# Optimization experiments

Hardware: AMD Instinct MI355X
Metric: run time of the kernel (lower is better)

Reference implementation:

```python
import jax, jax.numpy as jnp
import numpy as np

N = 50000      # num nodes
E = 800000     # num edges (avg degree 16)
IN = 128       # raw node feature dim
H = 64         # h_dim
L = 2          # num_conv
K = 5          # negative_rate
EPS = 1e-3     # keras BatchNormalization default epsilon


def setup_inputs() -> dict:
    key = jax.random.key(0)
    ks = jax.random.split(key, 12)
    node_feat = jax.random.normal(ks[0], (N, IN), dtype=jnp.float32)
    emb_w = jax.random.normal(ks[1], (IN, H), dtype=jnp.float32) * 0.05
    emb_b = jnp.zeros((H,), dtype=jnp.float32)
    conv_w = jax.random.normal(ks[2], (L, 2 * H, H), dtype=jnp.float32) * 0.05
    conv_b = jnp.zeros((L, H), dtype=jnp.float32)
    bn_gamma = 1.0 + 0.1 * jax.random.normal(ks[3], (L, H), dtype=jnp.float32)
    bn_beta = 0.1 * jax.random.normal(ks[4], (L, H), dtype=jnp.float32)
    bn_mean = 0.1 * jax.random.normal(ks[5], (L, H), dtype=jnp.float32)
    bn_var = jax.random.uniform(ks[6], (L, H), dtype=jnp.float32, minval=0.5, maxval=1.5)
    w_relation = jax.random.normal(ks[7], (1, H), dtype=jnp.float32) * 0.05
    src = jax.random.randint(ks[8], (E,), 0, N, dtype=jnp.int32)
    dst = jax.random.randint(ks[9], (E,), 0, N, dtype=jnp.int32)
    neg_dst = jax.random.randint(ks[10], (E * K,), 0, N, dtype=jnp.int32)
    return dict(node_feat=node_feat, emb_w=emb_w, emb_b=emb_b, conv_w=conv_w,
                conv_b=conv_b, bn_gamma=bn_gamma, bn_beta=bn_beta,
                bn_mean=bn_mean, bn_var=bn_var, w_relation=w_relation,
                src=src, dst=dst, neg_dst=neg_dst)


def reference(node_feat, emb_w, emb_b, conv_w, conv_b, bn_gamma, bn_beta,
              bn_mean, bn_var, w_relation, src, dst, neg_dst):
    # embedding layer (Dense)
    h = node_feat @ emb_w + emb_b  # [N, H]
    for i in range(L):
        # edge message: concat(h[src], h[dst]) @ W + b, split W to avoid [E,2H] buffer
        w_s, w_d = conv_w[i, :H], conv_w[i, H:]
        edge_feat = h[src] @ w_s + h[dst] @ w_d + conv_b[i]  # [E, H]
        # scatter-sum messages to destination nodes (zeros for isolated nodes)
        agg = jax.ops.segment_sum(edge_feat, dst, num_segments=N)  # [N, H]
        # node update: sigmoid(msg) + softplus(h)
        h = jax.nn.sigmoid(agg) + jax.nn.softplus(h)
        # BatchNormalization (inference: moving stats), then relu; dropout inactive
        h = bn_gamma[i] * (h - bn_mean[i]) * jax.lax.rsqrt(bn_var[i] + EPS) + bn_beta[i]
        h = jax.nn.relu(h)
    # link scoring: sum(h_u * h_v * w_relation)
    pos_scores = jnp.sum(h[src] * h[dst] * w_relation, axis=1)  # [E]
    neg_src = jnp.repeat(src, K)  # [E*K]
    # scatter-reorder in original is the identity permutation (pos_e_ids == arange(E))
    neg_scores = jnp.sum(h[neg_src] * h[neg_dst] * w_relation, axis=1)  # [E*K]
    return pos_scores, neg_scores
```

## Files before the change

kernel.cpp:

```cpp
#include <hip/hip_runtime.h>
#include <hip/hip_fp16.h>

#define NV 50000
#define EV 800000
#define INF 128
#define HD 64
#define KNEG 5
#define NB ((NV + 1023) / 1024)

#if defined(__has_builtin)
#if __has_builtin(__builtin_amdgcn_fdot2)
#define HAS_FDOT2 1
#endif
#endif

typedef _Float16 half2r __attribute__((ext_vector_type(2)));

__device__ __forceinline__ float dot2acc(unsigned a, unsigned b, float c) {
#ifdef HAS_FDOT2
  return __builtin_amdgcn_fdot2(__builtin_bit_cast(half2r, a),
                                __builtin_bit_cast(half2r, b), c, false);
#else
  const __half2 ha = *(const __half2*)&a;
  const __half2 hb = *(const __half2*)&b;
  return c + __low2float(ha) * __low2float(hb)
           + __high2float(ha) * __high2float(hb);
#endif
}

__device__ __forceinline__ unsigned packh2(float lo, float hi) {
  return __builtin_bit_cast(unsigned, __floats2half2_rn(lo, hi));
}

__global__ __launch_bounds__(256) void embed_kernel(
    const float* __restrict__ feat, const float* __restrict__ W,
    const float* __restrict__ b, __half* __restrict__ h) {
  __shared__ unsigned sF[4][2][256];
  const int lane = threadIdx.x & 63;
  const int wave = threadIdx.x >> 6;
  unsigned Wh[64];
#pragma unroll
  for (int j = 0; j < 64; j++)
    Wh[j] = packh2(W[(2 * j) * HD + lane], W[(2 * j + 1) * HD + lane]);
  const float bias = b[lane];
  const int nwaves = gridDim.x * 4;
  const int wid = blockIdx.x * 4 + wave;
  const int ngroups = NV / 4;

  int buf = 0;
  int g = wid;
  if (g < ngroups) {
    const float4* gp = (const float4*)(feat + (size_t)g * 512);
    const float4 a0 = gp[lane];
    const float4 a1 = gp[lane + 64];
    uint2 c0, c1;
    c0.x = packh2(a0.x, a0.y); c0.y = packh2(a0.z, a0.w);
    c1.x = packh2(a1.x, a1.y); c1.y = packh2(a1.z, a1.w);
    ((uint2*)sF[wave][0])[lane] = c0;
    ((uint2*)sF[wave][0])[lane + 64] = c1;
  }
  for (; g < ngroups; g += nwaves) {
    const int gn = g + nwaves;
    float4 b0, b1;
    if (gn < ngroups) {
      const float4* gp = (const float4*)(feat + (size_t)gn * 512);
      b0 = gp[lane];
      b1 = gp[lane + 64];
    }
    float acc0 = bias, acc1 = bias, acc2 = bias, acc3 = bias;
    const uint4* F = (const uint4*)sF[wave][buf];
#pragma unroll
    for (int t = 0; t < 16; t++) {
      const uint4 x0 = F[t];
      const uint4 x1 = F[16 + t];
      const uint4 x2 = F[32 + t];
      const uint4 x3 = F[48 + t];
      const unsigned w0 = Wh[4 * t + 0];
      const unsigned w1 = Wh[4 * t + 1];
      const unsigned w2 = Wh[4 * t + 2];
      const unsigned w3 = Wh[4 * t + 3];
      acc0 = dot2acc(x0.x, w0, acc0); acc0 = dot2acc(x0.y, w1, acc0);
      acc0 = dot2acc(x0.z, w2, acc0); acc0 = dot2acc(x0.w, w3, acc0);
      acc1 = dot2acc(x1.x, w0, acc1); acc1 = dot2acc(x1.y, w1, acc1);
      acc1 = dot2acc(x1.z, w2, acc1); acc1 = dot2acc(x1.w, w3, acc1);
      acc2 = dot2acc(x2.x, w0, acc2); acc2 = dot2acc(x2.y, w1, acc2);
      acc2 = dot2acc(x2.z, w2, acc2); acc2 = dot2acc(x2.w, w3, acc2);
      acc3 = dot2acc(x3.x, w0, acc3); acc3 = dot2acc(x3.y, w1, acc3);
      acc3 = dot2acc(x3.z, w2, acc3); acc3 = dot2acc(x3.w, w3, acc3);
    }
    __half* hpo = h + (size_t)g * 256 + lane;
    hpo[0]   = __float2half_rn(acc0);
    hpo[64]  = __float2half_rn(acc1);
    hpo[128] = __float2half_rn(acc2);
    hpo[192] = __float2half_rn(acc3);
    if (gn < ngroups) {
      uint2 c0, c1;
      c0.x = packh2(b0.x, b0.y); c0.y = packh2(b0.z, b0.w);
      c1.x = packh2(b1.x, b1.y); c1.y = packh2(b1.z, b1.w);
      ((uint2*)sF[wave][buf ^ 1])[lane] = c0;
      ((uint2*)sF[wave][buf ^ 1])[lane + 64] = c1;
      buf ^= 1;
    }
  }
}

__global__ __launch_bounds__(256) void hist_kernel(
    const int* __restrict__ dst, int* __restrict__ deg,
    unsigned short* __restrict__ rank) {
  const int e = blockIdx.x * 256 + threadIdx.x;
  if (e < EV) {
    const int r = atomicAdd(&deg[dst[e]], 1);
    rank[e] = (unsigned short)r;
  }
}

__global__ __launch_bounds__(1024) void scan_part_kernel(
    const int* __restrict__ deg, int* __restrict__ off,
    int* __restrict__ bsum) {
  __shared__ int wsum[16];
  const int tid = threadIdx.x;
  const int lane = tid & 63;
  const int w = tid >> 6;
  const int i = blockIdx.x * 1024 + tid;
  const int v = (i < NV) ? deg[i] : 0;
  int s = v;
#pragma unroll
  for (int ofs = 1; ofs < 64; ofs <<= 1) {
    int x = __shfl_up(s, ofs, 64);
    if (lane >= ofs) s += x;
  }
  if (lane == 63) wsum[w] = s;
  __syncthreads();
  if (w == 0) {
    int t2 = (lane < 16) ? wsum[lane] : 0;
#pragma unroll
    for (int ofs = 1; ofs < 16; ofs <<= 1) {
      int x = __shfl_up(t2, ofs, 64);
      if (lane >= ofs) t2 += x;
    }
    if (lane < 16) wsum[lane] = t2;
  }
  __syncthreads();
  const int base = (w > 0) ? wsum[w - 1] : 0;
  if (i < NV) off[i] = base + s - v;
  if (tid == 0) bsum[blockIdx.x] = wsum[15];
}

__global__ __launch_bounds__(1024) void scan_fix_kernel(
    const int* __restrict__ bsum, int* __restrict__ off) {
  __shared__ int sbase, stot;
  const int tid = threadIdx.x;
  const int b = blockIdx.x;
  if (tid == 0) {
    int acc = 0, tot = 0;
    for (int j = 0; j < NB; j++) {
      const int x = bsum[j];
      if (j < b) acc += x;
      tot += x;
    }
    sbase = acc;
    stot = tot;
  }
  __syncthreads();
  const int i = b * 1024 + tid;
  if (i < NV) off[i] += sbase;
  if (b == NB - 1 && tid == 0) off[NV] = stot;
}

__global__ __launch_bounds__(256) void perm_kernel(
    const int* __restrict__ src, const int* __restrict__ dst,
    const unsigned short* __restrict__ rank, const int* __restrict__ off,
    unsigned short* __restrict__ gsrc) {
  const int e = blockIdx.x * 256 + threadIdx.x;
  if (e < EV) {
    const int pos = off[dst[e]] + (int)rank[e];
    __builtin_nontemporal_store((unsigned short)src[e], &gsrc[pos]);
  }
}

__global__ __launch_bounds__(256) void aggcomb_kernel(
    const __half* __restrict__ hin, __half* __restrict__ hout,
    const unsigned short* __restrict__ gsrc, const int* __restrict__ off,
    const float* __restrict__ wconv, const float* __restrict__ cb,
    const float* __restrict__ gamma, const float* __restrict__ beta,
    const float* __restrict__ mean, const float* __restrict__ var) {
  __shared__ float sS1[4][4][HD];
  __shared__ float sH[4][4][HD];
  const int wave = threadIdx.x >> 6;
  const int lane = threadIdx.x & 63;
  const int sub = lane >> 4;
  const int q = lane & 15;
  const int f = lane;
  float Wsr[HD], Wdr[HD];
#pragma unroll
  for (int k = 0; k < HD; k++) Wsr[k] = wconv[k * HD + f];
#pragma unroll
  for (int k = 0; k < HD; k++) Wdr[k] = wconv[(HD + k) * HD + f];
  const float cbf = cb[f];
  const float gf = gamma[f];
  const float btf = beta[f];
  const float mf = mean[f];
  const float inv = rsqrtf(var[f] + 1e-3f);
  const uint2* hp = (const uint2*)hin;
  const int wid = blockIdx.x * 4 + wave;
  const int nw = gridDim.x * 4;
  const int ngroups = NV / 4;
  for (int g = wid; g < ngroups; g += nw) {
    const int n0 = g * 4;
    const int n = n0 + sub;
    const int j0 = off[n];
    const int deg = off[n + 1] - j0;
    int dm = deg;
    dm = max(dm, __shfl_xor(dm, 16, 64));
    dm = max(dm, __shfl_xor(dm, 32, 64));
    const uint2 hrv = hp[(size_t)n * 16 + q];
    float4 acc = make_float4(0.f, 0.f, 0.f, 0.f);
    for (int base = 0; base < dm; base += 16) {
      const int e = base + q;
      const int eid = (e < deg) ? (int)gsrc[j0 + e] : -1;
#pragma unroll
      for (int i = 0; i < 16; i++) {
        const int a = __shfl(eid, (sub << 4) | i, 64);
        const uint2 v = hp[(size_t)max(a, 0) * 16 + q];
        const __half2 p0 = *(const __half2*)&v.x;
        const __half2 p1 = *(const __half2*)&v.y;
        const float msk = (a >= 0) ? 1.f : 0.f;
        acc.x = fmaf(__low2float(p0),  msk, acc.x);
        acc.y = fmaf(__high2float(p0), msk, acc.y);
        acc.z = fmaf(__low2float(p1),  msk, acc.z);
        acc.w = fmaf(__high2float(p1), msk, acc.w);
      }
    }
    {
      const __half2 p0 = *(const __half2*)&hrv.x;
      const __half2 p1 = *(const __half2*)&hrv.y;
      const float4 hrowf = make_float4(__low2float(p0), __high2float(p0),
                                       __low2float(p1), __high2float(p1));
      ((float4*)sS1[wave][sub])[q] = acc;
      ((float4*)sH[wave][sub])[q] = hrowf;
    }
#pragma unroll
    for (int m4 = 0; m4 < 4; m4++) {
      const float4* s1p = (const float4*)sS1[wave][m4];
      const float4* hq = (const float4*)sH[wave][m4];
      float a1a = 0.f, a1b = 0.f, a2a = 0.f, a2b = 0.f;
#pragma unroll
      for (int k4 = 0; k4 < 16; k4++) {
        const float4 sv = s1p[k4];
        const float4 hv = hq[k4];
        a1a = fmaf(sv.x, Wsr[4 * k4 + 0], a1a);
        a1b = fmaf(sv.y, Wsr[4 * k4 + 1], a1b);
        a1a = fmaf(sv.z, Wsr[4 * k4 + 2], a1a);
        a1b = fmaf(sv.w, Wsr[4 * k4 + 3], a1b);
        a2a = fmaf(hv.x, Wdr[4 * k4 + 0], a2a);
        a2b = fmaf(hv.y, Wdr[4 * k4 + 1], a2b);
        a2a = fmaf(hv.z, Wdr[4 * k4 + 2], a2a);
        a2b = fmaf(hv.w, Wdr[4 * k4 + 3], a2b);
      }
      const float a1 = a1a + a1b;
      const float a2 = a2a + a2b;
      const float hvf = sH[wave][m4][f];
      const float d = (float)__shfl(deg, m4 << 4, 64);
      const float agg = a1 + d * a2 + d * cbf;
      const float sig = 1.f / (1.f + __expf(-agg));
      const float sp = fmaxf(hvf, 0.f) + log1pf(__expf(-fabsf(hvf)));
      float x = sig + sp;
      x = gf * (x - mf) * inv + btf;
      hout[(size_t)(n0 + m4) * HD + f] = __float2half_rn(fmaxf(x, 0.f));
    }
  }
}

__global__ __launch_bounds__(256) void score_kernel(
    const __half* __restrict__ hh, const int* __restrict__ src,
    const int* __restrict__ dst, const int* __restrict__ neg_dst,
    const float* __restrict__ wrel, float* __restrict__ out) {
  const int tid = blockIdx.x * 256 + threadIdx.x;
  const int e = tid >> 3;
  const int q = tid & 7;
  if (e >= EV) return;
  const float4 w0 = ((const float4*)wrel)[2 * q];
  const float4 w1 = ((const float4*)wrel)[2 * q + 1];
  const __half2 wh0 = __floats2half2_rn(w0.x, w0.y);
  const __half2 wh1 = __floats2half2_rn(w0.z, w0.w);
  const __half2 wh2 = __floats2half2_rn(w1.x, w1.y);
  const __half2 wh3 = __floats2half2_rn(w1.z, w1.w);
  const int s = src[e];
  const int d = dst[e];
  int nd[KNEG];
#pragma unroll
  for (int r = 0; r < KNEG; r++) nd[r] = neg_dst[e * KNEG + r];

  const uint4* hp = (const uint4*)hh;
  const uint4 sv = hp[(size_t)s * 8 + q];
  const uint4 dv = hp[(size_t)d * 8 + q];
  uint4 nv[KNEG];
#pragma unroll
  for (int r = 0; r < KNEG; r++) nv[r] = hp[(size_t)nd[r] * 8 + q];

  const unsigned au0 = __builtin_bit_cast(unsigned,
      __hmul2(*(const __half2*)&sv.x, wh0));
  const unsigned au1 = __builtin_bit_cast(unsigned,
      __hmul2(*(const __half2*)&sv.y, wh1));
  const unsigned au2 = __builtin_bit_cast(unsigned,
      __hmul2(*(const __half2*)&sv.z, wh2));
  const unsigned au3 = __builtin_bit_cast(unsigned,
      __hmul2(*(const __half2*)&sv.w, wh3));

  float v0 = dot2acc(au3, dv.w,
             dot2acc(au2, dv.z,
             dot2acc(au1, dv.y,
             dot2acc(au0, dv.x, 0.f))));
  float v1, v2, v3, v4, v5;
  {
    float pn[KNEG];
#pragma unroll
    for (int r = 0; r < KNEG; r++) {
      pn[r] = dot2acc(au3, nv[r].w,
              dot2acc(au2, nv[r].z,
              dot2acc(au1, nv[r].y,
              dot2acc(au0, nv[r].x, 0.f))));
    }
    v1 = pn[0]; v2 = pn[1]; v3 = pn[2]; v4 = pn[3]; v5 = pn[4];
  }
  {
    const bool hi = (q & 4) != 0;
    float t0 = hi ? v0 : v4, t1 = hi ? v1 : v5;
    float t2 = hi ? v2 : 0.f, t3 = hi ? v3 : 0.f;
    t0 = __shfl_xor(t0, 4, 64); t1 = __shfl_xor(t1, 4, 64);
    t2 = __shfl_xor(t2, 4, 64); t3 = __shfl_xor(t3, 4, 64);
    v0 = (hi ? v4 : v0) + t0;
    v1 = (hi ? v5 : v1) + t1;
    v2 = (hi ? 0.f : v2) + t2;
    v3 = (hi ? 0.f : v3) + t3;
  }
  {
    const bool hi = (q & 2) != 0;
    float t0 = hi ? v0 : v2, t1 = hi ? v1 : v3;
    t0 = __shfl_xor(t0, 2, 64); t1 = __shfl_xor(t1, 2, 64);
    v0 = (hi ? v2 : v0) + t0;
    v1 = (hi ? v3 : v1) + t1;
  }
  {
    const bool hi = (q & 1) != 0;
    float t0 = hi ? v0 : v1;
    t0 = __shfl_xor(t0, 1, 64);
    v0 = (hi ? v1 : v0) + t0;
  }
  if (q == 0) out[e] = v0;
  else if (q <= KNEG) out[(size_t)EV + (size_t)e * KNEG + (q - 1)] = v0;
}

extern "C" void kernel_launch(void* const* d_in, const int* in_sizes, int n_in,
                              void* d_out, int out_size, void* d_ws, size_t ws_size,
                              hipStream_t stream) {
  const float* node_feat = (const float*)d_in[0];
  const float* emb_w     = (const float*)d_in[1];
  const float* emb_b     = (const float*)d_in[2];
  const float* conv_w    = (const float*)d_in[3];
  const float* conv_b    = (const float*)d_in[4];
  const float* bn_gamma  = (const float*)d_in[5];
  const float* bn_beta   = (const float*)d_in[6];
  const float* bn_mean   = (const float*)d_in[7];
  const float* bn_var    = (const float*)d_in[8];
  const float* w_rel     = (const float*)d_in[9];
  const int*   src       = (const int*)d_in[10];
  const int*   dst       = (const int*)d_in[11];
  const int*   neg_dst   = (const int*)d_in[12];
  float* out = (float*)d_out;

  __half* H0 = (__half*)d_ws;
  __half* H1 = H0 + (size_t)NV * HD;
  int*   off  = (int*)(H1 + (size_t)NV * HD);
  unsigned short* gsrc = (unsigned short*)(off + (NV + 1));
  int*   bsum = (int*)(gsrc + EV);
  int*   deg  = (int*)H1;
  unsigned short* rank = (unsigned short*)(((int*)H1) + NV);

  hipMemsetAsync(deg, 0, (size_t)NV * sizeof(int), stream);
  hist_kernel<<<(EV + 255) / 256, 256, 0, stream>>>(dst, deg, rank);
  embed_kernel<<<1024, 256, 0, stream>>>(node_feat, emb_w, emb_b, H0);
  scan_part_kernel<<<NB, 1024, 0, stream>>>(deg, off, bsum);
  scan_fix_kernel<<<NB, 1024, 0, stream>>>(bsum, off);
  perm_kernel<<<(EV + 255) / 256, 256, 0, stream>>>(src, dst, rank, off, gsrc);

  aggcomb_kernel<<<512, 256, 0, stream>>>(
      H0, H1, gsrc, off, conv_w, conv_b,
      bn_gamma, bn_beta, bn_mean, bn_var);
  aggcomb_kernel<<<512, 256, 0, stream>>>(
      H1, H0, gsrc, off, conv_w + 2 * HD * HD, conv_b + HD,
      bn_gamma + HD, bn_beta + HD, bn_mean + HD, bn_var + HD);

  score_kernel<<<((size_t)EV * 8 + 255) / 256, 256, 0, stream>>>(
      H0, src, dst, neg_dst, w_rel, out);
}
```

Before: 315.7 us.

## Fuse histogram into embed kernel, use fp16 dot2 in node update, pad zero row

The degree histogram now runs as a grid-stride loop at the end of the embedding kernel, so one launch is dropped. The aggregation kernel replaces masked gathers with a padded all-zero sentinel row (index NV), which removes the mask multiply and the max() clamp. Its per-node matvec now uses packed fp16 weights with fdot2 on half-precision shared-memory staging, halving weight registers and LDS traffic. In exchange the summed neighbour features are rounded to fp16 before the matvec, which could overflow or lose precision, and two extra small memsets are added.

```diff
diff --git a/kernel.cpp b/kernel.cpp
--- a/kernel.cpp
+++ b/kernel.cpp
@@ -32,9 +32,11 @@
   return __builtin_bit_cast(unsigned, __floats2half2_rn(lo, hi));
 }
 
-__global__ __launch_bounds__(256) void embed_kernel(
+__global__ __launch_bounds__(256) void embed_hist_kernel(
     const float* __restrict__ feat, const float* __restrict__ W,
-    const float* __restrict__ b, __half* __restrict__ h) {
+    const float* __restrict__ b, __half* __restrict__ h,
+    const int* __restrict__ dst, int* __restrict__ deg,
+    unsigned short* __restrict__ rank) {
   __shared__ unsigned sF[4][2][256];
   const int lane = threadIdx.x & 63;
   const int wave = threadIdx.x >> 6;
@@ -102,13 +104,7 @@
       buf ^= 1;
     }
   }
-}
-
-__global__ __launch_bounds__(256) void hist_kernel(
-    const int* __restrict__ dst, int* __restrict__ deg,
-    unsigned short* __restrict__ rank) {
-  const int e = blockIdx.x * 256 + threadIdx.x;
-  if (e < EV) {
+  for (int e = blockIdx.x * 256 + threadIdx.x; e < EV; e += gridDim.x * 256) {
     const int r = atomicAdd(&deg[dst[e]], 1);
     rank[e] = (unsigned short)r;
   }
@@ -184,18 +180,20 @@
     const float* __restrict__ wconv, const float* __restrict__ cb,
     const float* __restrict__ gamma, const float* __restrict__ beta,
     const float* __restrict__ mean, const float* __restrict__ var) {
-  __shared__ float sS1[4][4][HD];
-  __shared__ float sH[4][4][HD];
+  __shared__ unsigned sS1[4][4][32];
+  __shared__ unsigned sH[4][4][32];
   const int wave = threadIdx.x >> 6;
   const int lane = threadIdx.x & 63;
   const int sub = lane >> 4;
   const int q = lane & 15;
   const int f = lane;
-  float Wsr[HD], Wdr[HD];
-#pragma unroll
-  for (int k = 0; k < HD; k++) Wsr[k] = wconv[k * HD + f];
-#pragma unroll
-  for (int k = 0; k < HD; k++) Wdr[k] = wconv[(HD + k) * HD + f];
+  unsigned Ws2[32], Wd2[32];
+#pragma unroll
+  for (int j = 0; j < 32; j++) {
+    Ws2[j] = packh2(wconv[(2 * j) * HD + f], wconv[(2 * j + 1) * HD + f]);
+    Wd2[j] = packh2(wconv[(HD + 2 * j) * HD + f],
+                    wconv[(HD + 2 * j + 1) * HD + f]);
+  }
   const float cbf = cb[f];
   const float gf = gamma[f];
   const float btf = beta[f];
@@ -217,49 +215,48 @@
     float4 acc = make_float4(0.f, 0.f, 0.f, 0.f);
     for (int base = 0; base < dm; base += 16) {
       const int e = base + q;
-      const int eid = (e < deg) ? (int)gsrc[j0 + e] : -1;
+      const int eid = (e < deg) ? (int)gsrc[j0 + e] : NV;
 #pragma unroll
       for (int i = 0; i < 16; i++) {
         const int a = __shfl(eid, (sub << 4) | i, 64);
-        const uint2 v = hp[(size_t)max(a, 0) * 16 + q];
+        const uint2 v = hp[(size_t)a * 16 + q];
         const __half2 p0 = *(const __half2*)&v.x;
         const __half2 p1 = *(const __half2*)&v.y;
-        const float msk = (a >= 0) ? 1.f : 0.f;
-        acc.x = fmaf(__low2float(p0),  msk, acc.x);
-        acc.y = fmaf(__high2float(p0), msk, acc.y);
-        acc.z = fmaf(__low2float(p1),  msk, acc.z);
-        acc.w = fmaf(__high2float(p1), msk, acc.w);
+        acc.x += __low2float(p0);
+        acc.y += __high2float(p0);
+        acc.z += __low2float(p1);
+        acc.w += __high2float(p1);
       }
     }
     {
-      const __half2 p0 = *(const __half2*)&hrv.x;
-      const __half2 p1 = *(const __half2*)&hrv.y;
-      const float4 hrowf = make_float4(__low2float(p0), __high2float(p0),
-                                       __low2float(p1), __high2float(p1));
-      ((float4*)sS1[wave][sub])[q] = acc;
-      ((float4*)sH[wave][sub])[q] = hrowf;
+      uint2 s1p;
+      s1p.x = packh2(acc.x, acc.y);
+      s1p.y = packh2(acc.z, acc.w);
+      ((uint2*)sS1[wave][sub])[q] = s1p;
+      ((uint2*)sH[wave][sub])[q] = hrv;
     }
 #pragma unroll
     for (int m4 = 0; m4 < 4; m4++) {
-      const float4* s1p = (const float4*)sS1[wave][m4];
-      const float4* hq = (const float4*)sH[wave][m4];
+      const uint4* s1p = (const uint4*)sS1[wave][m4];
+      const uint4* hq = (const uint4*)sH[wave][m4];
       float a1a = 0.f, a1b = 0.f, a2a = 0.f, a2b = 0.f;
 #pragma unroll
-      for (int k4 = 0; k4 < 16; k4++) {
-        const float4 sv = s1p[k4];
-        const float4 hv = hq[k4];
-        a1a = fmaf(sv.x, Wsr[4 * k4 + 0], a1a);
-        a1b = fmaf(sv.y, Wsr[4 * k4 + 1], a1b);
-        a1a = fmaf(sv.z, Wsr[4 * k4 + 2], a1a);
-        a1b = fmaf(sv.w, Wsr[4 * k4 + 3], a1b);
-        a2a = fmaf(hv.x, Wdr[4 * k4 + 0], a2a);
-        a2b = fmaf(hv.y, Wdr[4 * k4 + 1], a2b);
-        a2a = fmaf(hv.z, Wdr[4 * k4 + 2], a2a);
-        a2b = fmaf(hv.w, Wdr[4 * k4 + 3], a2b);
+      for (int t = 0; t < 8; t++) {
+        const uint4 xs = s1p[t];
+        const uint4 xh = hq[t];
+        a1a = dot2acc(xs.x, Ws2[4 * t + 0], a1a);
+        a1b = dot2acc(xs.y, Ws2[4 * t + 1], a1b);
+        a1a = dot2acc(xs.z, Ws2[4 * t + 2], a1a);
+        a1b = dot2acc(xs.w, Ws2[4 * t + 3], a1b);
+        a2a = dot2acc(xh.x, Wd2[4 * t + 0], a2a);
+        a2b = dot2acc(xh.y, Wd2[4 * t + 1], a2b);
+        a2a = dot2acc(xh.z, Wd2[4 * t + 2], a2a);
+        a2b = dot2acc(xh.w, Wd2[4 * t + 3], a2b);
       }
       const float a1 = a1a + a1b;
       const float a2 = a2a + a2b;
-      const float hvf = sH[wave][m4][f];
+      const float hvf =
+          __half2float(((const __half*)sH[wave][m4])[f]);
       const float d = (float)__shfl(deg, m4 << 4, 64);
       const float agg = a1 + d * a2 + d * cbf;
       const float sig = 1.f / (1.f + __expf(-agg));
@@ -370,16 +367,18 @@
   float* out = (float*)d_out;
 
   __half* H0 = (__half*)d_ws;
-  __half* H1 = H0 + (size_t)NV * HD;
-  int*   off  = (int*)(H1 + (size_t)NV * HD);
+  __half* H1 = H0 + (size_t)(NV + 1) * HD;
+  int*   off  = (int*)(H1 + (size_t)(NV + 1) * HD);
   unsigned short* gsrc = (unsigned short*)(off + (NV + 1));
   int*   bsum = (int*)(gsrc + EV);
   int*   deg  = (int*)H1;
-  unsigned short* rank = (unsigned short*)(((int*)H1) + NV);
+  unsigned short* rank = ((unsigned short*)H1) + 2 * NV;
 
   hipMemsetAsync(deg, 0, (size_t)NV * sizeof(int), stream);
-  hist_kernel<<<(EV + 255) / 256, 256, 0, stream>>>(dst, deg, rank);
-  embed_kernel<<<1024, 256, 0, stream>>>(node_feat, emb_w, emb_b, H0);
+  hipMemsetAsync(H0 + (size_t)NV * HD, 0, HD * sizeof(__half), stream);
+  hipMemsetAsync(H1 + (size_t)NV * HD, 0, HD * sizeof(__half), stream);
+  embed_hist_kernel<<<1024, 256, 0, stream>>>(node_feat, emb_w, emb_b, H0,
+                                              dst, deg, rank);
   scan_part_kernel<<<NB, 1024, 0, stream>>>(deg, off, bsum);
   scan_fix_kernel<<<NB, 1024, 0, stream>>>(bsum, off);
   perm_kernel<<<(EV + 255) / 256, 256, 0, stream>>>(src, dst, rank, off, gsrc);
```

Result: faster. 305.9 us (-3.1%).
